# Kernel optimization log

Hardware: AMD Instinct MI355X
Metric: run time of the kernel (lower is better)

Reference implementation:

```python
import jax, jax.numpy as jnp
import numpy as np

N, E = 100000, 400000
IN_DIM, PAD_DIM, HID = 384, 3, 64

def _xavier(key, fan_in, fan_out, shape=None):
    shape = shape or (fan_in, fan_out)
    lim = float(np.sqrt(6.0 / (fan_in + fan_out)))
    return jax.random.uniform(key, shape, jnp.float32, -lim, lim)

def setup_inputs():
    key = jax.random.key(0)
    ks = jax.random.split(key, 20)
    return {
        "x": jax.random.normal(ks[0], (N, IN_DIM), jnp.float32),
        "edge_index": jax.random.randint(ks[1], (2, E), 0, N),
        "pad_state": jax.random.uniform(ks[2], (PAD_DIM,), jnp.float32, -1.0, 1.0),
        # GAT layer 1: in = IN_DIM+PAD_DIM, heads=4, out=HID per head
        "W1": _xavier(ks[3], IN_DIM + PAD_DIM, 4 * HID),
        "att_src1": _xavier(ks[4], HID, HID, (4, HID)),
        "att_dst1": _xavier(ks[5], HID, HID, (4, HID)),
        "b1": jnp.zeros((4 * HID,), jnp.float32),
        # GAT layer 2: in = 4*HID, heads=2
        "W2": _xavier(ks[6], 4 * HID, 2 * HID),
        "att_src2": _xavier(ks[7], HID, HID, (2, HID)),
        "att_dst2": _xavier(ks[8], HID, HID, (2, HID)),
        "b2": jnp.zeros((2 * HID,), jnp.float32),
        # attention-score MLP
        "aw1": _xavier(ks[9], 2 * HID, HID),
        "ab1": jnp.zeros((HID,), jnp.float32),
        "aw2": _xavier(ks[10], HID, 1),
        "ab2": jnp.zeros((1,), jnp.float32),
        # emotion gate
        "gw": _xavier(ks[11], PAD_DIM, HID),
        "gb": jnp.zeros((HID,), jnp.float32),
    }

def _gat(h_in, src, dst, W, a_src, a_dst, bias, heads):
    # PyG GATConv (eval mode): linear -> per-head LeakyReLU attention logits
    # -> edge softmax over destination -> scatter-add aggregation -> concat heads + bias
    n = h_in.shape[0]
    h = (h_in @ W).reshape(n, heads, -1)               # [N,H,C]
    al_s = jnp.einsum('nhc,hc->nh', h, a_src)          # [N,H]
    al_d = jnp.einsum('nhc,hc->nh', h, a_dst)
    e = jax.nn.leaky_relu(al_s[src] + al_d[dst], 0.2)  # [Etot,H]
    m = jax.ops.segment_max(e, dst, num_segments=n)    # stable softmax per dst
    p = jnp.exp(e - m[dst])
    denom = jax.ops.segment_sum(p, dst, num_segments=n)
    coef = p / (denom[dst] + 1e-16)
    out = jax.ops.segment_sum(h[src] * coef[:, :, None], dst, num_segments=n)
    return out.reshape(n, -1) + bias

def reference(x, edge_index, pad_state, W1, att_src1, att_dst1, b1,
              W2, att_src2, att_dst2, b2, aw1, ab1, aw2, ab2, gw, gb):
    n = x.shape[0]
    loops = jnp.arange(n, dtype=edge_index.dtype)      # add_self_loops=True default
    src = jnp.concatenate([edge_index[0], loops])
    dst = jnp.concatenate([edge_index[1], loops])
    pad_exp = jnp.broadcast_to(pad_state.reshape(1, -1), (n, pad_state.size))
    h = jnp.concatenate([x, pad_exp], axis=-1)         # [N, in_dim+pad_dim]
    h = jax.nn.elu(_gat(h, src, dst, W1, att_src1, att_dst1, b1, 4))
    h = jax.nn.elu(_gat(h, src, dst, W2, att_src2, att_dst2, b2, 2))
    gate = jax.nn.sigmoid(pad_exp @ gw + gb)           # [N,HID]
    h = h * jnp.tile(gate, (1, 2))                     # [N,2*HID]
    attn = jax.nn.sigmoid(jax.nn.relu(h @ aw1 + ab1) @ aw2 + ab2)  # [N,1]
    return h, attn
```

## Files before the change

### kernel.cpp

```cpp
#include <hip/hip_runtime.h>
#include <hip/hip_bf16.h>
#include <stdint.h>

#define IN_DIM 384
#define HID 64
#define C1 256
#define C2 128

typedef unsigned int uint32;
typedef __bf16 bf16x8 __attribute__((ext_vector_type(8)));
typedef float f32x4 __attribute__((ext_vector_type(4)));

static __device__ __forceinline__ float bf2f(unsigned short u){
    return __uint_as_float(((uint32)u) << 16);
}
static __device__ __forceinline__ unsigned short f2bf(float x){
    uint32 u = __float_as_uint(x);
    return (unsigned short)((u + 0x7FFFu + ((u >> 16) & 1u)) >> 16);
}
static __device__ __forceinline__ uint32 pack2(float a, float b){
    return (uint32)f2bf(a) | ((uint32)f2bf(b) << 16);
}

__global__ void k_zero(int* deg, int* cur, int N){
    int i = blockIdx.x*256 + threadIdx.x;
    if (i < N){ deg[i] = 0; cur[i] = 0; }
}
__global__ void k_hist(const int* __restrict__ ei, int* deg, int E){
    int i = blockIdx.x*256 + threadIdx.x;
    if (i < E) atomicAdd(&deg[ei[E + i]], 1);
}
__global__ void k_scan1(const int* __restrict__ deg, int* rowptr, int* part, int N){
    __shared__ int s[256];
    int tid = threadIdx.x;
    int i = blockIdx.x*256 + tid;
    int v = (i < N) ? deg[i] : 0;
    s[tid] = v; __syncthreads();
    for (int off = 1; off < 256; off <<= 1){
        int t = (tid >= off) ? s[tid - off] : 0;
        __syncthreads();
        s[tid] += t;
        __syncthreads();
    }
    if (i < N) rowptr[i] = s[tid] - v;
    if (tid == 255) part[blockIdx.x] = s[tid];
}
__global__ void k_scan2(int* part, int nb){
    __shared__ int s[512];
    int tid = threadIdx.x;
    int v = (tid < nb) ? part[tid] : 0;
    s[tid] = v; __syncthreads();
    for (int off = 1; off < 512; off <<= 1){
        int t = (tid >= off) ? s[tid - off] : 0;
        __syncthreads();
        s[tid] += t;
        __syncthreads();
    }
    if (tid < nb) part[tid] = s[tid] - v;
}
__global__ void k_scan3(int* rowptr, const int* __restrict__ part, int N, int E){
    int i = blockIdx.x*256 + threadIdx.x;
    if (i < N) rowptr[i] += part[blockIdx.x];
    if (i == 0) rowptr[N] = E;
}
__global__ void k_scatter(const int* __restrict__ ei, const int* __restrict__ rowptr,
                          int* cur, int* colx, int* dstx, int E){
    int i = blockIdx.x*256 + threadIdx.x;
    if (i < E){
        int d = ei[E + i];
        int pos = atomicAdd(&cur[d], 1);
        int p = rowptr[d] + pos;
        colx[p] = ei[i];
        dstx[p] = d;
    }
}

__global__ __launch_bounds__(256) void k_cvtW(const float* __restrict__ W,
        unsigned short* __restrict__ Wf, int ncol, int ntiles, int nunits){
    int unit = blockIdx.x*4 + (threadIdx.x >> 6);
    if (unit >= nunits) return;
    int l = threadIdx.x & 63;
    int s = unit / ntiles, ct = unit % ntiles;
    int col = ct*16 + (l & 15);
    int g = l >> 4;
    unsigned short o[8];
    #pragma unroll
    for (int j = 0; j < 8; j++){
        int k = s*32 + g*8 + j;
        o[j] = f2bf(W[(size_t)k*ncol + col]);
    }
    ushort4* dst = (ushort4*)&Wf[((size_t)unit*64 + l)*8];
    dst[0] = make_ushort4(o[0], o[1], o[2], o[3]);
    dst[1] = make_ushort4(o[4], o[5], o[6], o[7]);
}

__global__ __launch_bounds__(256) void k_cvtX(const float* __restrict__ x,
        unsigned short* __restrict__ xs, int N){
    const int blk = blockIdx.x;
    const int n0  = blk*64;
    const int t   = threadIdx.x;
    unsigned short* dst = xs + (size_t)blk*24576;
    const bool full = (n0 + 64 <= N);
    #pragma unroll
    for (int it = 0; it < 24; ++it){
        int flat = it*256 + t;
        int row  = flat / 96;
        int k4   = flat - row*96;
        int k    = k4*4;
        const float* src;
        if (full){
            src = x + (size_t)n0*IN_DIM + (size_t)flat*4;
        } else {
            int n = n0 + row; if (n > N-1) n = N-1;
            src = x + (size_t)n*IN_DIM + k;
        }
        float4 a = *(const float4*)src;
        int ku   = k >> 5;
        int l16  = (k >> 3) & 3;
        int half = (k >> 2) & 1;
        int lane = l16*16 + (row & 15);
        int rt   = row >> 4;
        int chunk = (ku*4 + rt)*64 + lane;
        *(uint2*)(dst + (size_t)chunk*8 + half*4) = make_uint2(pack2(a.x, a.y), pack2(a.z, a.w));
    }
}

__global__ __launch_bounds__(256) void k_prep(const float* __restrict__ W1,
        const float* __restrict__ pad, const float* __restrict__ gw, const float* __restrict__ gb,
        float* __restrict__ c1v, float* __restrict__ gate){
    int tid = threadIdx.x;
    c1v[tid] = pad[0]*W1[(size_t)(IN_DIM+0)*C1 + tid]
             + pad[1]*W1[(size_t)(IN_DIM+1)*C1 + tid]
             + pad[2]*W1[(size_t)(IN_DIM+2)*C1 + tid];
    if (tid < HID){
        float g = pad[0]*gw[0*HID + tid] + pad[1]*gw[1*HID + tid] + pad[2]*gw[2*HID + tid] + gb[tid];
        gate[tid] = 1.f/(1.f + __expf(-g));
    }
}

__global__ __launch_bounds__(512) void k_gemm1_mfma(const unsigned short* __restrict__ xs,
        const unsigned short* __restrict__ Wf, const float* __restrict__ c1v,
        const float* __restrict__ as1, const float* __restrict__ ad1,
        unsigned short* __restrict__ h1, float* __restrict__ als, float* __restrict__ ald, int N)
{
    __shared__ unsigned short Af[3072*8];
    const int tid = threadIdx.x;
    const int l   = tid & 63;
    const int w   = tid >> 6;
    const int wr  = w >> 2;
    const int wc  = w & 3;
    const int n0  = blockIdx.x * 64;

    const unsigned short* src = xs + (size_t)blockIdx.x*24576;
    uint4 st[6];
    #pragma unroll
    for (int j = 0; j < 6; j++) st[j] = *(const uint4*)(src + (size_t)(j*512 + tid)*8);
    #pragma unroll
    for (int j = 0; j < 6; j++) *(uint4*)&Af[(size_t)(j*512 + tid)*8] = st[j];

    f32x4 acc[4][2];
    #pragma unroll
    for (int i = 0; i < 4; i++)
        #pragma unroll
        for (int rt = 0; rt < 2; rt++)
            acc[i][rt] = (f32x4){0.f, 0.f, 0.f, 0.f};

    uint4 wcur[4], wnxt[4];
    {
        const unsigned short* p = Wf + ((size_t)(wc*4)*64 + l)*8;
        #pragma unroll
        for (int i = 0; i < 4; i++) wcur[i] = *(const uint4*)(p + (size_t)i*512);
    }
    __syncthreads();

    for (int ku = 0; ku < 12; ++ku){
        if (ku < 11){
            const unsigned short* p = Wf + ((size_t)((ku+1)*16 + wc*4)*64 + l)*8;
            #pragma unroll
            for (int i = 0; i < 4; i++) wnxt[i] = *(const uint4*)(p + (size_t)i*512);
        }
        bf16x8 af[2];
        #pragma unroll
        for (int rt = 0; rt < 2; rt++)
            af[rt] = __builtin_bit_cast(bf16x8, *(const uint4*)&Af[((ku*4 + wr*2 + rt)*64 + l)*8]);
        #pragma unroll
        for (int i = 0; i < 4; i++){
            bf16x8 bw = __builtin_bit_cast(bf16x8, wcur[i]);
            #pragma unroll
            for (int rt = 0; rt < 2; rt++)
                acc[i][rt] = __builtin_amdgcn_mfma_f32_16x16x32_bf16(bw, af[rt], acc[i][rt], 0, 0, 0);
        }
        if (ku < 11){
            #pragma unroll
            for (int i = 0; i < 4; i++) wcur[i] = wnxt[i];
        }
    }

    const int g = l >> 4;
    float4 cvv[4], av[4], dv[4];
    #pragma unroll
    for (int i = 0; i < 4; i++){
        int cl = i*16 + g*4;
        cvv[i] = *(const float4*)&c1v[wc*64 + cl];
        av[i]  = *(const float4*)&as1[wc*64 + cl];
        dv[i]  = *(const float4*)&ad1[wc*64 + cl];
    }
    #pragma unroll
    for (int rt = 0; rt < 2; rt++){
        int node = n0 + (wr*2 + rt)*16 + (l & 15);
        bool ok = node < N;
        float ps = 0.f, pd = 0.f;
        #pragma unroll
        for (int i = 0; i < 4; i++){
            float h0 = acc[i][rt][0] + cvv[i].x;
            float h1v = acc[i][rt][1] + cvv[i].y;
            float h2v = acc[i][rt][2] + cvv[i].z;
            float h3v = acc[i][rt][3] + cvv[i].w;
            ps += h0*av[i].x + h1v*av[i].y + h2v*av[i].z + h3v*av[i].w;
            pd += h0*dv[i].x + h1v*dv[i].y + h2v*dv[i].z + h3v*dv[i].w;
            if (ok){
                ushort4 o = make_ushort4(f2bf(h0), f2bf(h1v), f2bf(h2v), f2bf(h3v));
                *(ushort4*)&h1[(size_t)node*C1 + wc*64 + i*16 + g*4] = o;
            }
        }
        ps += __shfl_xor(ps, 16, 64); ps += __shfl_xor(ps, 32, 64);
        pd += __shfl_xor(pd, 16, 64); pd += __shfl_xor(pd, 32, 64);
        if (ok && g == 0){
            als[(size_t)node*4 + wc] = ps;
            ald[(size_t)node*4 + wc] = pd;
        }
    }
}

__global__ __launch_bounds__(256) void k_gemm2_mfma(const unsigned short* __restrict__ x2,
        const unsigned short* __restrict__ Wf,
        const float* __restrict__ as2, const float* __restrict__ ad2,
        unsigned short* __restrict__ h2, float* __restrict__ als, float* __restrict__ ald, int N)
{
    __shared__ unsigned short Af[2][4*64*8];
    const int tid = threadIdx.x;
    const int l   = tid & 63;
    const int w   = tid >> 6;
    const int wr  = w >> 1, wc = w & 1;
    const int n0  = blockIdx.x * 64;

    const int sr  = tid >> 2;
    const int kc  = tid & 3;
    const int d0  = ((sr >> 4)*64 + kc*16 + (sr & 15))*8;
    int crow = n0 + sr; if (crow > N-1) crow = N-1;
    const unsigned short* xrow = x2 + (size_t)crow*C1 + kc*8;

    f32x4 acc[4][2];
    #pragma unroll
    for (int i = 0; i < 4; i++)
        #pragma unroll
        for (int rt = 0; rt < 2; rt++)
            acc[i][rt] = (f32x4){0.f, 0.f, 0.f, 0.f};

    uint4 p0, wcur[4], wnxt[4];
    p0 = *(const uint4*)(xrow);
    *(uint4*)&Af[0][d0] = p0;
    {
        const unsigned short* p = Wf + ((size_t)(wc*4)*64 + l)*8;
        #pragma unroll
        for (int i = 0; i < 4; i++) wcur[i] = *(const uint4*)(p + (size_t)i*512);
    }
    __syncthreads();

    for (int s = 0; s < 8; ++s){
        if (s < 7){
            p0 = *(const uint4*)(xrow + (s+1)*32);
            const unsigned short* p = Wf + ((size_t)((s+1)*8 + wc*4)*64 + l)*8;
            #pragma unroll
            for (int i = 0; i < 4; i++) wnxt[i] = *(const uint4*)(p + (size_t)i*512);
        }
        bf16x8 af[2];
        #pragma unroll
        for (int rt = 0; rt < 2; rt++)
            af[rt] = __builtin_bit_cast(bf16x8, *(const uint4*)&Af[s&1][((wr*2 + rt)*64 + l)*8]);
        #pragma unroll
        for (int i = 0; i < 4; i++){
            bf16x8 bw = __builtin_bit_cast(bf16x8, wcur[i]);
            #pragma unroll
            for (int rt = 0; rt < 2; rt++)
                acc[i][rt] = __builtin_amdgcn_mfma_f32_16x16x32_bf16(bw, af[rt], acc[i][rt], 0, 0, 0);
        }
        if (s < 7){
            *(uint4*)&Af[(s+1)&1][d0] = p0;
            __syncthreads();
            #pragma unroll
            for (int i = 0; i < 4; i++) wcur[i] = wnxt[i];
        }
    }

    const int g = l >> 4;
    float4 av[4], dv[4];
    #pragma unroll
    for (int i = 0; i < 4; i++){
        int cl = i*16 + g*4;
        av[i] = *(const float4*)&as2[wc*64 + cl];
        dv[i] = *(const float4*)&ad2[wc*64 + cl];
    }
    #pragma unroll
    for (int rt = 0; rt < 2; rt++){
        int node = n0 + wr*32 + rt*16 + (l & 15);
        bool ok = node < N;
        float ps = 0.f, pd = 0.f;
        #pragma unroll
        for (int i = 0; i < 4; i++){
            float h0 = acc[i][rt][0], h1v = acc[i][rt][1];
            float h2v = acc[i][rt][2], h3v = acc[i][rt][3];
            ps += h0*av[i].x + h1v*av[i].y + h2v*av[i].z + h3v*av[i].w;
            pd += h0*dv[i].x + h1v*dv[i].y + h2v*dv[i].z + h3v*dv[i].w;
            if (ok){
                ushort4 o = make_ushort4(f2bf(h0), f2bf(h1v), f2bf(h2v), f2bf(h3v));
                *(ushort4*)&h2[(size_t)node*C2 + wc*64 + i*16 + g*4] = o;
            }
        }
        ps += __shfl_xor(ps, 16, 64); ps += __shfl_xor(ps, 32, 64);
        pd += __shfl_xor(pd, 16, 64); pd += __shfl_xor(pd, 32, 64);
        if (ok && g == 0){
            als[(size_t)node*2 + wc] = ps;
            ald[(size_t)node*2 + wc] = pd;
        }
    }
}

template<int H>
__global__ __launch_bounds__(256) void k_elogit(const int* __restrict__ colx,
        const int* __restrict__ dstx, const float* __restrict__ als,
        const float* __restrict__ ald, float* __restrict__ ep, int E)
{
    int i = blockIdx.x*256 + threadIdx.x;
    if (i >= E) return;
    int s = colx[i], d = dstx[i];
    if constexpr (H == 4){
        float4 a = *(const float4*)&als[(size_t)s*4];
        float4 b = *(const float4*)&ald[(size_t)d*4];
        float4 e;
        e.x = a.x + b.x; e.x = fmaxf(e.x, 0.2f*e.x);
        e.y = a.y + b.y; e.y = fmaxf(e.y, 0.2f*e.y);
        e.z = a.z + b.z; e.z = fmaxf(e.z, 0.2f*e.z);
        e.w = a.w + b.w; e.w = fmaxf(e.w, 0.2f*e.w);
        *(float4*)&ep[(size_t)i*4] = e;
    } else {
        float2 a = *(const float2*)&als[(size_t)s*2];
        float2 b = *(const float2*)&ald[(size_t)d*2];
        float2 e;
        e.x = a.x + b.x; e.x = fmaxf(e.x, 0.2f*e.x);
        e.y = a.y + b.y; e.y = fmaxf(e.y, 0.2f*e.y);
        *(float2*)&ep[(size_t)i*2] = e;
    }
}

template<int H>
__global__ __launch_bounds__(256) void k_segsm(const int* __restrict__ rowptr,
        const float* __restrict__ als, const float* __restrict__ ald,
        float* __restrict__ ep, float* __restrict__ den, float* __restrict__ pSelf, int NH)
{
    int t = blockIdx.x*256 + threadIdx.x;
    if (t >= NH) return;
    int node = t / H;
    int head = t - node*H;
    int base = rowptr[node];
    int cnt  = rowptr[node+1] - base;
    float es = als[t] + ald[t];
    es = fmaxf(es, 0.2f*es);
    float m = es;
    for (int j = 0; j < cnt; j++)
        m = fmaxf(m, ep[(size_t)(base + j)*H + head]);
    float ps = __expf(es - m);
    float dn = ps;
    for (int j = 0; j < cnt; j++){
        size_t idx = (size_t)(base + j)*H + head;
        float p = __expf(ep[idx] - m);
        ep[idx] = p;
        dn += p;
    }
    den[t]   = dn;
    pSelf[t] = ps;
}

template<int H, int CPL, int LAYER>
__global__ __launch_bounds__(256) void k_gat(const unsigned short* __restrict__ hlin,
        const float* __restrict__ ep, const float* __restrict__ den, const float* __restrict__ pSelf,
        const int* __restrict__ rowptr, const int* __restrict__ colx,
        const float* __restrict__ bias, const float* __restrict__ gate,
        unsigned short* __restrict__ out_bf, float* __restrict__ out_f, int N)
{
    constexpr int C = H*64;
    constexpr uint32 RB = C*2;
    int lane = threadIdx.x & 63, wid = threadIdx.x >> 6;
    int n = blockIdx.x*4 + wid;
    if (n >= N) return;
    const int c0 = lane*CPL;
    const int head = c0 >> 6;
    const int base = rowptr[n];
    const int cnt  = rowptr[n+1] - base;
    const char* hbase = (const char*)hlin + (uint32)c0*2;

    float acc[CPL];
    {
        float psf = pSelf[(uint32)n*H + head];
        if constexpr (CPL == 4){
            ushort4 v = *(const ushort4*)(hbase + (size_t)(uint32)n*RB);
            acc[0] = psf*bf2f(v.x); acc[1] = psf*bf2f(v.y);
            acc[2] = psf*bf2f(v.z); acc[3] = psf*bf2f(v.w);
        } else {
            uint32 v = *(const uint32*)(hbase + (size_t)(uint32)n*RB);
            acc[0] = psf*bf2f((unsigned short)(v & 0xffff));
            acc[1] = psf*bf2f((unsigned short)(v >> 16));
        }
    }
    for (int i = 0; i < cnt; i += 4){
        int idx[4], sk[4];
        #pragma unroll
        for (int k = 0; k < 4; k++){
            int ii = i + k; if (ii > cnt-1) ii = cnt-1;
            idx[k] = base + ii;
        }
        #pragma unroll
        for (int k = 0; k < 4; k++) sk[k] = colx[idx[k]];
        float pk[4];
        #pragma unroll
        for (int k = 0; k < 4; k++){
            float pv = ep[(size_t)(uint32)idx[k]*H + head];
            pk[k] = (i + k < cnt) ? pv : 0.f;
        }
        if constexpr (CPL == 4){
            ushort4 h4[4];
            #pragma unroll
            for (int k = 0; k < 4; k++) h4[k] = *(const ushort4*)(hbase + (size_t)(uint32)sk[k]*RB);
            #pragma unroll
            for (int k = 0; k < 4; k++){
                acc[0] += pk[k]*bf2f(h4[k].x);
                acc[1] += pk[k]*bf2f(h4[k].y);
                acc[2] += pk[k]*bf2f(h4[k].z);
                acc[3] += pk[k]*bf2f(h4[k].w);
            }
        } else {
            uint32 h2v[4];
            #pragma unroll
            for (int k = 0; k < 4; k++) h2v[k] = *(const uint32*)(hbase + (size_t)(uint32)sk[k]*RB);
            #pragma unroll
            for (int k = 0; k < 4; k++){
                acc[0] += pk[k]*bf2f((unsigned short)(h2v[k] & 0xffff));
                acc[1] += pk[k]*bf2f((unsigned short)(h2v[k] >> 16));
            }
        }
    }

    float inv = 1.f/(den[(uint32)n*H + head] + 1e-16f);
    if constexpr (LAYER == 1){
        unsigned short o[CPL];
        #pragma unroll
        for (int j = 0; j < CPL; j++){
            float r = acc[j]*inv + bias[c0 + j];
            r = (r > 0.f) ? r : (__expf(r) - 1.f);
            o[j] = f2bf(r);
        }
        if constexpr (CPL == 4){
            ushort4 ov; ov.x = o[0]; ov.y = o[1]; ov.z = o[2]; ov.w = o[3];
            *(ushort4*)&out_bf[(size_t)n*C + c0] = ov;
        }
    } else {
        float o[CPL];
        #pragma unroll
        for (int j = 0; j < CPL; j++){
            float r = acc[j]*inv + bias[c0 + j];
            r = (r > 0.f) ? r : (__expf(r) - 1.f);
            o[j] = r*gate[(c0 + j) & 63];
        }
        if constexpr (CPL == 2){
            *(float2*)&out_f[(size_t)n*C + c0] = make_float2(o[0], o[1]);
        }
    }
}

__global__ __launch_bounds__(256) void k_attn_mfma(const float* __restrict__ outh,
        const unsigned short* __restrict__ Wfa, const float* __restrict__ ab1,
        const float* __restrict__ aw2, const float* __restrict__ ab2,
        float* __restrict__ attn, int N)
{
    __shared__ unsigned short Af[4*8*64*8];
    const int tid = threadIdx.x;
    const int l   = tid & 63;
    const int w   = tid >> 6;
    const int n0  = blockIdx.x * 128;

    const int r  = tid >> 1;
    const int kh = tid & 1;
    const int rt8 = r >> 4, rr = r & 15;
    int crow = n0 + r; if (crow > N-1) crow = N-1;
    const float* src = outh + (size_t)crow*C2 + kh*16;
    #pragma unroll
    for (int s = 0; s < 4; s++){
        float4 a = *(const float4*)(src + s*32 + 0);
        float4 b = *(const float4*)(src + s*32 + 4);
        float4 c = *(const float4*)(src + s*32 + 8);
        float4 d = *(const float4*)(src + s*32 + 12);
        uint4 u0, u1;
        u0.x = pack2(a.x, a.y); u0.y = pack2(a.z, a.w);
        u0.z = pack2(b.x, b.y); u0.w = pack2(b.z, b.w);
        u1.x = pack2(c.x, c.y); u1.y = pack2(c.z, c.w);
        u1.z = pack2(d.x, d.y); u1.w = pack2(d.z, d.w);
        int d0 = ((s*8 + rt8)*64 + (kh*2)*16 + rr)*8;
        *(uint4*)&Af[d0]       = u0;
        *(uint4*)&Af[d0 + 128] = u1;
    }
    __syncthreads();

    f32x4 acc[4][2];
    #pragma unroll
    for (int i = 0; i < 4; i++)
        #pragma unroll
        for (int rt = 0; rt < 2; rt++)
            acc[i][rt] = (f32x4){0.f, 0.f, 0.f, 0.f};

    #pragma unroll
    for (int s = 0; s < 4; s++){
        bf16x8 af[2];
        #pragma unroll
        for (int rt = 0; rt < 2; rt++)
            af[rt] = __builtin_bit_cast(bf16x8, *(const uint4*)&Af[((s*8 + w*2 + rt)*64 + l)*8]);
        #pragma unroll
        for (int i = 0; i < 4; i++){
            bf16x8 bw = __builtin_bit_cast(bf16x8, *(const uint4*)&Wfa[((size_t)(s*4 + i)*64 + l)*8]);
            #pragma unroll
            for (int rt = 0; rt < 2; rt++)
                acc[i][rt] = __builtin_amdgcn_mfma_f32_16x16x32_bf16(bw, af[rt], acc[i][rt], 0, 0, 0);
        }
    }

    const int g = l >> 4;
    float4 abv[4], awv[4];
    #pragma unroll
    for (int i = 0; i < 4; i++){
        abv[i] = *(const float4*)&ab1[i*16 + g*4];
        awv[i] = *(const float4*)&aw2[i*16 + g*4];
    }
    float b2v = ab2[0];
    #pragma unroll
    for (int rt = 0; rt < 2; rt++){
        int node = n0 + (w*2 + rt)*16 + (l & 15);
        float part = 0.f;
        #pragma unroll
        for (int i = 0; i < 4; i++){
            float v0 = fmaxf(acc[i][rt][0] + abv[i].x, 0.f);
            float v1 = fmaxf(acc[i][rt][1] + abv[i].y, 0.f);
            float v2 = fmaxf(acc[i][rt][2] + abv[i].z, 0.f);
            float v3 = fmaxf(acc[i][rt][3] + abv[i].w, 0.f);
            part += v0*awv[i].x + v1*awv[i].y + v2*awv[i].z + v3*awv[i].w;
        }
        part += __shfl_xor(part, 16, 64);
        part += __shfl_xor(part, 32, 64);
        if (g == 0 && node < N)
            attn[node] = 1.f/(1.f + __expf(-(part + b2v)));
    }
}

extern "C" void kernel_launch(void* const* d_in, const int* in_sizes, int n_in,
                              void* d_out, int out_size, void* d_ws, size_t ws_size,
                              hipStream_t stream)
{
    const float* x    = (const float*)d_in[0];
    const int*   ei   = (const int*)  d_in[1];
    const float* pad  = (const float*)d_in[2];
    const float* W1   = (const float*)d_in[3];
    const float* as1  = (const float*)d_in[4];
    const float* ad1  = (const float*)d_in[5];
    const float* b1   = (const float*)d_in[6];
    const float* W2   = (const float*)d_in[7];
    const float* as2  = (const float*)d_in[8];
    const float* ad2  = (const float*)d_in[9];
    const float* b2   = (const float*)d_in[10];
    const float* aw1  = (const float*)d_in[11];
    const float* ab1  = (const float*)d_in[12];
    const float* aw2  = (const float*)d_in[13];
    const float* ab2  = (const float*)d_in[14];
    const float* gw   = (const float*)d_in[15];
    const float* gb   = (const float*)d_in[16];

    const int N = in_sizes[0] / IN_DIM;
    const int E = in_sizes[1] / 2;

    float* outh    = (float*)d_out;
    float* outattn = outh + (size_t)N*C2;

    char* w = (char*)d_ws;
    auto alloc = [&](size_t bytes)->char*{
        char* p = w;
        w += (bytes + 255) & ~(size_t)255;
        return p;
    };
    unsigned short* h1  = (unsigned short*)alloc((size_t)N*C1*2);
    unsigned short* x2  = (unsigned short*)alloc((size_t)N*C1*2);
    unsigned short* h2  = (unsigned short*)alloc((size_t)N*C2*2);
    char*           xpad= alloc(65536);
    float* als1 = (float*)alloc((size_t)N*4*4);
    float* ald1 = (float*)alloc((size_t)N*4*4);
    float* als2 = (float*)alloc((size_t)N*2*4);
    float* ald2 = (float*)alloc((size_t)N*2*4);
    int* deg    = (int*)alloc((size_t)N*4);
    int* cur    = (int*)alloc((size_t)N*4);
    int* rowptr = (int*)alloc((size_t)(N+1)*4);
    int* colx   = (int*)alloc((size_t)E*4);
    int* dstx   = (int*)alloc((size_t)E*4);
    int* part   = (int*)alloc(512*4);
    unsigned short* Wf1 = (unsigned short*)alloc((size_t)12*16*64*8*2);
    unsigned short* Wf2 = (unsigned short*)alloc((size_t)8*8*64*8*2);
    unsigned short* Wfa = (unsigned short*)alloc((size_t)4*4*64*8*2);
    float* c1v  = (float*)alloc(C1*4);
    float* gate = (float*)alloc(HID*4);
    (void)xpad;

    unsigned short* xs = x2;
    float* ep1    = (float*)h2;
    float* den1   = (float*)((char*)h2 + (size_t)E*16);
    float* pSelf1 = (float*)((char*)h2 + (size_t)E*16 + (size_t)N*16);
    float* ep2    = (float*)x2;
    float* den2   = (float*)((char*)x2 + (size_t)E*8);
    float* pSelf2 = (float*)((char*)x2 + (size_t)E*8 + (size_t)N*8);

    const int nbN = (N + 255)/256;
    const int nbE = (E + 255)/256;
    const int nbW = (N + 3)/4;
    const int nbG = (N + 63)/64;
    const int nbA = (N + 127)/128;

    k_cvtW <<<(192+3)/4, 256, 0, stream>>>(W1, Wf1, C1, 16, 192);
    k_cvtW <<<(64+3)/4,  256, 0, stream>>>(W2, Wf2, C2, 8, 64);
    k_cvtW <<<(16+3)/4,  256, 0, stream>>>(aw1, Wfa, HID, 4, 16);
    k_prep <<<1, 256, 0, stream>>>(W1, pad, gw, gb, c1v, gate);

    k_cvtX <<<nbG, 256, 0, stream>>>(x, xs, N);

    k_zero   <<<nbN, 256, 0, stream>>>(deg, cur, N);
    k_hist   <<<nbE, 256, 0, stream>>>(ei, deg, E);
    k_scan1  <<<nbN, 256, 0, stream>>>(deg, rowptr, part, N);
    k_scan2  <<<1, 512, 0, stream>>>(part, nbN);
    k_scan3  <<<nbN, 256, 0, stream>>>(rowptr, part, N, E);
    k_scatter<<<nbE, 256, 0, stream>>>(ei, rowptr, cur, colx, dstx, E);

    k_gemm1_mfma<<<nbG, 512, 0, stream>>>(xs, Wf1, c1v, as1, ad1, h1, als1, ald1, N);
    k_elogit<4><<<nbE, 256, 0, stream>>>(colx, dstx, als1, ald1, ep1, E);
    k_segsm<4> <<<(N*4 + 255)/256, 256, 0, stream>>>(rowptr, als1, ald1, ep1, den1, pSelf1, N*4);
    k_gat<4,4,1><<<nbW, 256, 0, stream>>>(h1, ep1, den1, pSelf1, rowptr, colx, b1,
                                          nullptr, x2, nullptr, N);

    k_gemm2_mfma<<<nbG, 256, 0, stream>>>(x2, Wf2, as2, ad2, h2, als2, ald2, N);
    k_elogit<2><<<nbE, 256, 0, stream>>>(colx, dstx, als2, ald2, ep2, E);
    k_segsm<2> <<<(N*2 + 255)/256, 256, 0, stream>>>(rowptr, als2, ald2, ep2, den2, pSelf2, N*2);
    k_gat<2,2,2><<<nbW, 256, 0, stream>>>(h2, ep2, den2, pSelf2, rowptr, colx, b2,
                                          gate, nullptr, outh, N);

    k_attn_mfma<<<nbA, 256, 0, stream>>>(outh, Wfa, ab1, aw2, ab2, outattn, N);
}
```

Before: 348.9 us.

## Fuse fp32-to-bf16 conversion of x into GEMM1 with swizzled LDS layout

Removes the separate k_cvtX pass that converted x to a bf16 fragment-ordered buffer. GEMM1 now loads fp32 x rows directly, packs them to bf16, and stores them into shared memory in row-major form with an XOR swizzle to avoid bank conflicts when reading MFMA fragments. This drops one kernel launch plus a full write and re-read of the 77 MB bf16 copy of x, at the cost of more registers per thread (12 float4 staging values) and more global load bytes inside the GEMM kernel.

```diff
diff --git a/kernel.cpp b/kernel.cpp
--- a/kernel.cpp
+++ b/kernel.cpp
@@ -94,37 +94,6 @@
     dst[1] = make_ushort4(o[4], o[5], o[6], o[7]);
 }
 
-__global__ __launch_bounds__(256) void k_cvtX(const float* __restrict__ x,
-        unsigned short* __restrict__ xs, int N){
-    const int blk = blockIdx.x;
-    const int n0  = blk*64;
-    const int t   = threadIdx.x;
-    unsigned short* dst = xs + (size_t)blk*24576;
-    const bool full = (n0 + 64 <= N);
-    #pragma unroll
-    for (int it = 0; it < 24; ++it){
-        int flat = it*256 + t;
-        int row  = flat / 96;
-        int k4   = flat - row*96;
-        int k    = k4*4;
-        const float* src;
-        if (full){
-            src = x + (size_t)n0*IN_DIM + (size_t)flat*4;
-        } else {
-            int n = n0 + row; if (n > N-1) n = N-1;
-            src = x + (size_t)n*IN_DIM + k;
-        }
-        float4 a = *(const float4*)src;
-        int ku   = k >> 5;
-        int l16  = (k >> 3) & 3;
-        int half = (k >> 2) & 1;
-        int lane = l16*16 + (row & 15);
-        int rt   = row >> 4;
-        int chunk = (ku*4 + rt)*64 + lane;
-        *(uint2*)(dst + (size_t)chunk*8 + half*4) = make_uint2(pack2(a.x, a.y), pack2(a.z, a.w));
-    }
-}
-
 __global__ __launch_bounds__(256) void k_prep(const float* __restrict__ W1,
         const float* __restrict__ pad, const float* __restrict__ gw, const float* __restrict__ gb,
         float* __restrict__ c1v, float* __restrict__ gate){
@@ -138,25 +107,44 @@
     }
 }
 
-__global__ __launch_bounds__(512) void k_gemm1_mfma(const unsigned short* __restrict__ xs,
+__global__ __launch_bounds__(512) void k_gemm1_mfma(const float* __restrict__ x,
         const unsigned short* __restrict__ Wf, const float* __restrict__ c1v,
         const float* __restrict__ as1, const float* __restrict__ ad1,
         unsigned short* __restrict__ h1, float* __restrict__ als, float* __restrict__ ald, int N)
 {
-    __shared__ unsigned short Af[3072*8];
+    __shared__ unsigned short Af[24576];
     const int tid = threadIdx.x;
     const int l   = tid & 63;
     const int w   = tid >> 6;
     const int wr  = w >> 2;
     const int wc  = w & 3;
     const int n0  = blockIdx.x * 64;
-
-    const unsigned short* src = xs + (size_t)blockIdx.x*24576;
-    uint4 st[6];
-    #pragma unroll
-    for (int j = 0; j < 6; j++) st[j] = *(const uint4*)(src + (size_t)(j*512 + tid)*8);
-    #pragma unroll
-    for (int j = 0; j < 6; j++) *(uint4*)&Af[(size_t)(j*512 + tid)*8] = st[j];
+    const bool full = (n0 + 64 <= N);
+
+    float4 rx[12];
+    if (full){
+        const float* bp = x + (size_t)n0*IN_DIM;
+        #pragma unroll
+        for (int it = 0; it < 12; ++it)
+            rx[it] = *(const float4*)(bp + (size_t)(it*512 + tid)*4);
+    } else {
+        #pragma unroll
+        for (int it = 0; it < 12; ++it){
+            int f = it*512 + tid;
+            int row = f/96, k4 = f - row*96;
+            int n = n0 + row; if (n > N-1) n = N-1;
+            rx[it] = *(const float4*)(x + (size_t)n*IN_DIM + k4*4);
+        }
+    }
+    #pragma unroll
+    for (int it = 0; it < 12; ++it){
+        uint32 f = (uint32)(it*512 + tid);
+        uint32 row = f/96;
+        uint32 byte = f*8;
+        uint32 swz = byte ^ ((row & 7) << 4);
+        uint2 v = make_uint2(pack2(rx[it].x, rx[it].y), pack2(rx[it].z, rx[it].w));
+        *(uint2*)((char*)Af + swz) = v;
+    }
 
     f32x4 acc[4][2];
     #pragma unroll
@@ -173,6 +161,13 @@
     }
     __syncthreads();
 
+    const uint32 frow0 = (uint32)((wr*2 + 0)*16 + (l & 15));
+    const uint32 frow1 = (uint32)((wr*2 + 1)*16 + (l & 15));
+    const uint32 fb0 = frow0*768 + ((uint32)(l >> 4) << 4);
+    const uint32 fb1 = frow1*768 + ((uint32)(l >> 4) << 4);
+    const uint32 fx0 = (frow0 & 7) << 4;
+    const uint32 fx1 = (frow1 & 7) << 4;
+
     for (int ku = 0; ku < 12; ++ku){
         if (ku < 11){
             const unsigned short* p = Wf + ((size_t)((ku+1)*16 + wc*4)*64 + l)*8;
@@ -180,9 +175,8 @@
             for (int i = 0; i < 4; i++) wnxt[i] = *(const uint4*)(p + (size_t)i*512);
         }
         bf16x8 af[2];
-        #pragma unroll
-        for (int rt = 0; rt < 2; rt++)
-            af[rt] = __builtin_bit_cast(bf16x8, *(const uint4*)&Af[((ku*4 + wr*2 + rt)*64 + l)*8]);
+        af[0] = __builtin_bit_cast(bf16x8, *(const uint4*)((char*)Af + ((fb0 + ku*64) ^ fx0)));
+        af[1] = __builtin_bit_cast(bf16x8, *(const uint4*)((char*)Af + ((fb1 + ku*64) ^ fx1)));
         #pragma unroll
         for (int i = 0; i < 4; i++){
             bf16x8 bw = __builtin_bit_cast(bf16x8, wcur[i]);
@@ -596,7 +590,6 @@
     unsigned short* h1  = (unsigned short*)alloc((size_t)N*C1*2);
     unsigned short* x2  = (unsigned short*)alloc((size_t)N*C1*2);
     unsigned short* h2  = (unsigned short*)alloc((size_t)N*C2*2);
-    char*           xpad= alloc(65536);
     float* als1 = (float*)alloc((size_t)N*4*4);
     float* ald1 = (float*)alloc((size_t)N*4*4);
     float* als2 = (float*)alloc((size_t)N*2*4);
@@ -612,9 +605,7 @@
     unsigned short* Wfa = (unsigned short*)alloc((size_t)4*4*64*8*2);
     float* c1v  = (float*)alloc(C1*4);
     float* gate = (float*)alloc(HID*4);
-    (void)xpad;
-
-    unsigned short* xs = x2;
+
     float* ep1    = (float*)h2;
     float* den1   = (float*)((char*)h2 + (size_t)E*16);
     float* pSelf1 = (float*)((char*)h2 + (size_t)E*16 + (size_t)N*16);
@@ -633,8 +624,6 @@
     k_cvtW <<<(16+3)/4,  256, 0, stream>>>(aw1, Wfa, HID, 4, 16);
     k_prep <<<1, 256, 0, stream>>>(W1, pad, gw, gb, c1v, gate);
 
-    k_cvtX <<<nbG, 256, 0, stream>>>(x, xs, N);
-
     k_zero   <<<nbN, 256, 0, stream>>>(deg, cur, N);
     k_hist   <<<nbE, 256, 0, stream>>>(ei, deg, E);
     k_scan1  <<<nbN, 256, 0, stream>>>(deg, rowptr, part, N);
@@ -642,7 +631,7 @@
     k_scan3  <<<nbN, 256, 0, stream>>>(rowptr, part, N, E);
     k_scatter<<<nbE, 256, 0, stream>>>(ei, rowptr, cur, colx, dstx, E);
 
-    k_gemm1_mfma<<<nbG, 512, 0, stream>>>(xs, Wf1, c1v, as1, ad1, h1, als1, ald1, N);
+    k_gemm1_mfma<<<nbG, 512, 0, stream>>>(x, Wf1, c1v, as1, ad1, h1, als1, ald1, N);
     k_elogit<4><<<nbE, 256, 0, stream>>>(colx, dstx, als1, ald1, ep1, E);
     k_segsm<4> <<<(N*4 + 255)/256, 256, 0, stream>>>(rowptr, als1, ald1, ep1, den1, pSelf1, N*4);
     k_gat<4,4,1><<<nbW, 256, 0, stream>>>(h1, ep1, den1, pSelf1, rowptr, colx, b1,
```

New measurement: 301.6 us. -13.6%, faster.
